# Kernel tuning notes

Measured on AMD Instinct MI355X. Metric: run time of the kernel, lower is better.

Reference implementation:

```python
import jax, jax.numpy as jnp
import numpy as np

NEG_INF = -9.0e15  # matches torch reference's -9e15 masking constant


def setup_inputs() -> dict:
    key = jax.random.key(0)
    k1, k2, k3, k4 = jax.random.split(key, 4)
    N, F_IN, F_OUT = 8192, 256, 256
    x = jax.random.normal(k1, (N, F_IN), dtype=jnp.float32)
    adj = jax.random.randint(k2, (N, N), 0, 2, dtype=jnp.int32)
    W = jax.random.normal(k3, (F_OUT, F_IN), dtype=jnp.float32) * (1.0 / np.sqrt(F_IN))
    a = jax.random.normal(k4, (2 * F_OUT,), dtype=jnp.float32) * (1.0 / np.sqrt(2 * F_OUT))
    return {"x": x, "adj": adj, "W": W, "a": a}


def reference(x, adj, W, a):
    # h = W x  -> [N, F_OUT]
    h = x @ W.T
    F_OUT = h.shape[1]
    # The concat trick: e[i, j] = leaky_relu(a1 . h_i + a2 . h_j)
    # (repeat_interleave gives h_i as the first half, repeat gives h_j as the second half)
    a1, a2 = a[:F_OUT], a[F_OUT:]
    s_i = h @ a1  # [N] -- contribution of destination/row node i
    s_j = h @ a2  # [N] -- contribution of source/col node j
    e = jax.nn.leaky_relu(s_i[:, None] + s_j[None, :], negative_slope=0.2)  # [N, N]
    att = jnp.where(adj > 0, e, jnp.asarray(NEG_INF, dtype=e.dtype))
    att = jax.nn.softmax(att, axis=1)
    # dropout is identity in eval mode / for the deterministic reference
    h_prime = att @ h  # [N, F_OUT]
    return h_prime
```

## Files before the change

kernel.cpp:

```cpp
#include <hip/hip_runtime.h>
#include <hip/hip_bf16.h>

typedef __attribute__((ext_vector_type(4))) float f32x4;
typedef __attribute__((ext_vector_type(8))) short s16x8;
typedef __attribute__((ext_vector_type(4))) int i32x4;
typedef __attribute__((ext_vector_type(4))) unsigned short u16x4;

#define NEG_INF_F (-9.0e15f)
#define LOG2E_F 1.44269504088896340736f
#define N_ROWS 8192
#define F_DIM 256

__device__ __forceinline__ unsigned short f2bf(float f) {
    unsigned int u = __builtin_bit_cast(unsigned int, f);
    u += 0x7fffu + ((u >> 16) & 1u);
    return (unsigned short)(u >> 16);
}

__device__ __forceinline__ float fast_exp2(float x) {
#if __has_builtin(__builtin_amdgcn_exp2f)
    return __builtin_amdgcn_exp2f(x);
#else
    return exp2f(x);
#endif
}

__device__ __forceinline__ short f2bf_fast(float f) {
    __hip_bfloat16 b = __float2bfloat16(f);
    return __builtin_bit_cast(short, b);
}

__global__ __launch_bounds__(256) void k0_pack(const int* __restrict__ adj,
                                               unsigned* __restrict__ mask32) {
    const int t0 = (int)blockIdx.x * 256 + (int)threadIdx.x;
    const int nt = (int)gridDim.x * 256;
#pragma unroll 1
    for (int w = t0; w < (N_ROWS * N_ROWS / 32); w += nt) {
        const int* p = adj + (size_t)w * 32;
        unsigned m = 0;
#pragma unroll
        for (int i = 0; i < 8; ++i) {
            i32x4 v = *(const i32x4*)(p + i * 4);
            m |= (v[0] > 0 ? 1u : 0u) << (i * 4);
            m |= (v[1] > 0 ? 2u : 0u) << (i * 4);
            m |= (v[2] > 0 ? 4u : 0u) << (i * 4);
            m |= (v[3] > 0 ? 8u : 0u) << (i * 4);
        }
        mask32[w] = m;
    }
}

__global__ __launch_bounds__(256) void k1_gemm(const float* __restrict__ x,
                                               const float* __restrict__ W,
                                               unsigned short* __restrict__ hTp) {
    __shared__ float xT[128][64];
    __shared__ float wT[128][64];
    const int tid = threadIdx.x;
    const int rb = blockIdx.x >> 2, fbk = blockIdx.x & 3;
    const int row0 = rb * 64, f0 = fbk * 64;
    const int rs = tid >> 2, cs = tid & 3;
    const int r0 = (tid & 15) * 4, fc = (tid >> 4) * 4;
    float acc[4][4];
#pragma unroll
    for (int i = 0; i < 4; ++i)
#pragma unroll
        for (int j = 0; j < 4; ++j) acc[i][j] = 0.0f;

#pragma unroll 1
    for (int p = 0; p < 2; ++p) {
        const int kb = p * 128;
        if (p) __syncthreads();
        const float* xrow = x + (size_t)(row0 + rs) * F_DIM + kb + cs * 32;
        const float* wrow = W + (size_t)(f0 + rs) * F_DIM + kb + cs * 32;
#pragma unroll
        for (int i = 0; i < 8; ++i) {
            f32x4 xv = *(const f32x4*)(xrow + i * 4);
            f32x4 wv = *(const f32x4*)(wrow + i * 4);
#pragma unroll
            for (int jj = 0; jj < 4; ++jj) {
                xT[cs * 32 + i * 4 + jj][rs] = xv[jj];
                wT[cs * 32 + i * 4 + jj][rs] = wv[jj];
            }
        }
        __syncthreads();
#pragma unroll 4
        for (int kk = 0; kk < 128; ++kk) {
            f32x4 xv = *(const f32x4*)&xT[kk][r0];
            f32x4 wv = *(const f32x4*)&wT[kk][fc];
#pragma unroll
            for (int i = 0; i < 4; ++i)
#pragma unroll
                for (int j = 0; j < 4; ++j)
                    acc[i][j] = fmaf(xv[i], wv[j], acc[i][j]);
        }
    }
    const int kblk = (row0 + r0) >> 3, kslot = (row0 + r0) & 7;
#pragma unroll
    for (int j = 0; j < 4; ++j) {
        u16x4 t;
        t[0] = f2bf(acc[0][j]); t[1] = f2bf(acc[1][j]);
        t[2] = f2bf(acc[2][j]); t[3] = f2bf(acc[3][j]);
        *(u16x4*)(hTp + (size_t)kblk * 2048 + (f0 + fc + j) * 8 + kslot) = t;
    }
}

__global__ __launch_bounds__(256) void kva(const float* __restrict__ W,
                                           const float* __restrict__ a,
                                           float* __restrict__ va) {
    const int k = threadIdx.x;
    const int b = blockIdx.x;
    const float* av = a + b * 256;
    float s0 = 0.f, s1 = 0.f, s2 = 0.f, s3 = 0.f;
#pragma unroll 8
    for (int f = 0; f < 256; f += 4) {
        s0 = fmaf(av[f],     W[(size_t)f * 256 + k],       s0);
        s1 = fmaf(av[f + 1], W[(size_t)(f + 1) * 256 + k], s1);
        s2 = fmaf(av[f + 2], W[(size_t)(f + 2) * 256 + k], s2);
        s3 = fmaf(av[f + 3], W[(size_t)(f + 3) * 256 + k], s3);
    }
    va[b * 256 + k] = (s0 + s1) + (s2 + s3);
}

__global__ __launch_bounds__(256) void k1b_s(const float* __restrict__ x,
                                             const float* __restrict__ va,
                                             float* __restrict__ s1,
                                             float* __restrict__ s2) {
    const int tid = threadIdx.x, lane = tid & 63, w = tid >> 6;
    f32x4 a1 = *(const f32x4*)(va + lane * 4);
    f32x4 a2 = *(const f32x4*)(va + 256 + lane * 4);
    const int row0 = blockIdx.x * 32 + w * 8;
#pragma unroll 1
    for (int rr = 0; rr < 8; ++rr) {
        const int row = row0 + rr;
        f32x4 hv = *(const f32x4*)(x + (size_t)row * F_DIM + lane * 4);
        float p1 = hv[0] * a1[0] + hv[1] * a1[1] + hv[2] * a1[2] + hv[3] * a1[3];
        float p2 = hv[0] * a2[0] + hv[1] * a2[1] + hv[2] * a2[2] + hv[3] * a2[3];
#pragma unroll
        for (int o = 32; o; o >>= 1) { p1 += __shfl_xor(p1, o); p2 += __shfl_xor(p2, o); }
        if (lane == 0) { s1[row] = p1; s2[row] = p2; }
    }
}

__global__ __launch_bounds__(256) void kmax(const unsigned* __restrict__ mask32,
                                            const float* __restrict__ s2,
                                            float* __restrict__ Mrow) {
    __shared__ float s2l[8192];
    const int tid = threadIdx.x, lane = tid & 63, wv = tid >> 6;
#pragma unroll
    for (int i = 0; i < 8; ++i) {
        const int idx = (i * 256 + tid) * 4;
        *(f32x4*)&s2l[idx] = *(const f32x4*)(s2 + idx);
    }
    __syncthreads();
    const int row = (int)blockIdx.x * 4 + wv;
    const unsigned* __restrict__ mr = mask32 + (size_t)row * 256;
    float vmax = NEG_INF_F;
#pragma unroll 1
    for (int wi = 0; wi < 4; ++wi) {
        const unsigned m = mr[lane * 4 + wi];
        const int kb = (lane * 4 + wi) * 32;
#pragma unroll
        for (int cc = 0; cc < 8; ++cc) {
            const int c = (cc + lane) & 7;
            f32x4 v = *(const f32x4*)&s2l[kb + c * 4];
            const unsigned sh = (unsigned)(c * 4);
            vmax = fmaxf(vmax, ((m >> (sh + 0)) & 1u) ? v[0] : NEG_INF_F);
            vmax = fmaxf(vmax, ((m >> (sh + 1)) & 1u) ? v[1] : NEG_INF_F);
            vmax = fmaxf(vmax, ((m >> (sh + 2)) & 1u) ? v[2] : NEG_INF_F);
            vmax = fmaxf(vmax, ((m >> (sh + 3)) & 1u) ? v[3] : NEG_INF_F);
        }
    }
#pragma unroll
    for (int o = 32; o; o >>= 1) vmax = fmaxf(vmax, __shfl_xor(vmax, o));
    if (lane == 0) Mrow[row] = vmax;
}


#define P_ONE(D, SV, BIT, SI, MC)                                             \
    { float t_ = (SI) + (SV); t_ = fmaxf(t_, 0.2f * t_);                      \
      D = fast_exp2(fmaf(((bb_ & (BIT)) ? t_ : NEG_INF_F), LOG2E_F, -(MC))); }

#define RG_STEP(ACC, ACCL, BFR, MW, SI, MC)                                   \
    {                                                                         \
        const unsigned bb_ = ((MW) >> koff) & 0xffu;                          \
        float p0_, p1_, p2_, p3_, p4_, p5_, p6_, p7_;                         \
        P_ONE(p0_, svA_[0], 1u, SI, MC)   P_ONE(p1_, svA_[1], 2u, SI, MC)     \
        P_ONE(p2_, svA_[2], 4u, SI, MC)   P_ONE(p3_, svA_[3], 8u, SI, MC)     \
        P_ONE(p4_, svB_[0], 16u, SI, MC)  P_ONE(p5_, svB_[1], 32u, SI, MC)    \
        P_ONE(p6_, svB_[2], 64u, SI, MC)  P_ONE(p7_, svB_[3], 128u, SI, MC)   \
        s16x8 af_;                                                            \
        af_[0] = f2bf_fast(p0_); af_[1] = f2bf_fast(p1_);                     \
        af_[2] = f2bf_fast(p2_); af_[3] = f2bf_fast(p3_);                     \
        af_[4] = f2bf_fast(p4_); af_[5] = f2bf_fast(p5_);                     \
        af_[6] = f2bf_fast(p6_); af_[7] = f2bf_fast(p7_);                     \
        _Pragma("unroll")                                                     \
        for (int nt_ = 0; nt_ < 8; ++nt_)                                     \
            ACC[nt_] = __builtin_amdgcn_mfma_f32_16x16x32_bf16(af_, BFR[nt_], ACC[nt_], 0, 0, 0); \
        ACCL = __builtin_amdgcn_mfma_f32_16x16x32_bf16(af_, bones, ACCL, 0, 0, 0); \
    }

#define HALF_STEP(BFR, MWA, MWB, K)                                           \
    {                                                                         \
        const f32x4 svA_ = *(const f32x4*)(s2 + (K) + koff);                  \
        const f32x4 svB_ = *(const f32x4*)(s2 + (K) + koff + 4);              \
        RG_STEP(accA, accLA, BFR, MWA, siA, mCA)                              \
        RG_STEP(accB, accLB, BFR, MWB, siB, mCB)                              \
    }

#define LOAD_B(DST, K)                                                        \
    _Pragma("unroll")                                                         \
    for (int nt_ = 0; nt_ < 8; ++nt_)                                         \
        DST[nt_] = *(const s16x8*)(hTp + (unsigned)(((K) >> 3) + kg) * 2048u + vb + (unsigned)(nt_ * 128));

__global__ __launch_bounds__(256) void k2_attn(const unsigned* __restrict__ mask32,
                                               const unsigned short* __restrict__ hTp,
                                               const float* __restrict__ s1,
                                               const float* __restrict__ s2,
                                               const float* __restrict__ Mrow,
                                               float* __restrict__ out) {
    __shared__ float lbuf[4][2][16];
    __shared__ float accbuf[3][16][132];

    const int tid = threadIdx.x;
    const int lane = tid & 63;
    const int wc = tid >> 6;
    const int lane15 = lane & 15, kg = lane >> 4, koff = kg * 8;
    const int rowblk = (int)blockIdx.x >> 1;
    const int fh = (int)blockIdx.x & 1;
    const int row0 = rowblk * 32;
    const int mrowA = row0 + lane15, mrowB = row0 + 16 + lane15;
    const int fb = fh * 128;
    const int kbase = wc * 2048;
    const float siA = s1[mrowA], siB = s1[mrowB];
    const float tmxA = siA + Mrow[mrowA], tmxB = siB + Mrow[mrowB];
    const float mCA = fmaxf(tmxA, 0.2f * tmxA) * LOG2E_F;
    const float mCB = fmaxf(tmxB, 0.2f * tmxB) * LOG2E_F;
    const unsigned* __restrict__ mA32 = mask32 + (size_t)mrowA * 256;
    const unsigned* __restrict__ mB32 = mask32 + (size_t)mrowB * 256;

    f32x4 accA[8], accB[8], accLA, accLB;
#pragma unroll
    for (int nt = 0; nt < 8; ++nt) {
        f32x4 z = {0.f, 0.f, 0.f, 0.f};
        accA[nt] = z; accB[nt] = z;
    }
    { f32x4 z = {0.f, 0.f, 0.f, 0.f}; accLA = z; accLB = z; }

    s16x8 bones;
#pragma unroll
    for (int j = 0; j < 8; ++j) bones[j] = (short)0x3F80;

    const unsigned vb = (unsigned)(fb + lane15) * 8u;

    s16x8 bA[8], bB[8];
    LOAD_B(bA, kbase)
    unsigned mwA = mA32[kbase >> 5], mwB = mB32[kbase >> 5];

#pragma unroll 1
    for (int it = 0; it < 64; it += 2) {
        const int k0 = kbase + it * 32;
        const int k1 = k0 + 32;
        const int k2n = (it + 2 < 64) ? (k0 + 64) : kbase;

        LOAD_B(bB, k1)
        const unsigned mwnA = mA32[k1 >> 5], mwnB = mB32[k1 >> 5];

        HALF_STEP(bA, mwA, mwB, k0);

        LOAD_B(bA, k2n)
        mwA = mA32[k2n >> 5]; mwB = mB32[k2n >> 5];

        HALF_STEP(bB, mwnA, mwnB, k1);
    }

    if (lane15 == 0) {
#pragma unroll
        for (int r = 0; r < 4; ++r) {
            lbuf[wc][0][kg * 4 + r] = accLA[r];
            lbuf[wc][1][kg * 4 + r] = accLB[r];
        }
    }

    if (wc > 0) {
#pragma unroll
        for (int r = 0; r < 4; ++r)
#pragma unroll
            for (int nt = 0; nt < 8; ++nt)
                accbuf[wc - 1][kg * 4 + r][nt * 16 + lane15] = accA[nt][r];
    }
    __syncthreads();
    if (wc == 0) {
#pragma unroll
        for (int r = 0; r < 4; ++r) {
            const int dr = kg * 4 + r;
            const float lt = (lbuf[0][0][dr] + lbuf[1][0][dr]) + (lbuf[2][0][dr] + lbuf[3][0][dr]);
            const float inv = 1.0f / lt;
            float* orow_p = out + (size_t)(row0 + dr) * F_DIM + fb + lane15;
#pragma unroll
            for (int nt = 0; nt < 8; ++nt) {
                const float v = accA[nt][r] + accbuf[0][dr][nt * 16 + lane15]
                              + accbuf[1][dr][nt * 16 + lane15]
                              + accbuf[2][dr][nt * 16 + lane15];
                orow_p[nt * 16] = v * inv;
            }
        }
    }
    __syncthreads();

    if (wc > 0) {
#pragma unroll
        for (int r = 0; r < 4; ++r)
#pragma unroll
            for (int nt = 0; nt < 8; ++nt)
                accbuf[wc - 1][kg * 4 + r][nt * 16 + lane15] = accB[nt][r];
    }
    __syncthreads();
    if (wc == 0) {
#pragma unroll
        for (int r = 0; r < 4; ++r) {
            const int dr = kg * 4 + r;
            const float lt = (lbuf[0][1][dr] + lbuf[1][1][dr]) + (lbuf[2][1][dr] + lbuf[3][1][dr]);
            const float inv = 1.0f / lt;
            float* orow_p = out + (size_t)(row0 + 16 + dr) * F_DIM + fb + lane15;
#pragma unroll
            for (int nt = 0; nt < 8; ++nt) {
                const float v = accB[nt][r] + accbuf[0][dr][nt * 16 + lane15]
                              + accbuf[1][dr][nt * 16 + lane15]
                              + accbuf[2][dr][nt * 16 + lane15];
                orow_p[nt * 16] = v * inv;
            }
        }
    }
}

extern "C" void kernel_launch(void* const* d_in, const int* in_sizes, int n_in,
                              void* d_out, int out_size, void* d_ws, size_t ws_size,
                              hipStream_t stream) {
    (void)in_sizes; (void)n_in; (void)out_size; (void)ws_size;
    const float* x  = (const float*)d_in[0];
    const int*  adj = (const int*)d_in[1];
    const float* W  = (const float*)d_in[2];
    const float* a  = (const float*)d_in[3];
    float* out = (float*)d_out;
    char* ws = (char*)d_ws;
    unsigned short* hTp = (unsigned short*)ws;
    float* s1 = (float*)(ws + (4 << 20));
    float* s2 = (float*)(ws + (4 << 20) + (32 << 10));
    float* va = (float*)(ws + (4 << 20) + (64 << 10));
    float* Mr = (float*)(ws + (4 << 20) + (96 << 10));
    unsigned* mk = (unsigned*)(ws + (4 << 20) + (128 << 10));

    k0_pack<<<2048, 256, 0, stream>>>(adj, mk);
    k1_gemm<<<512, 256, 0, stream>>>(x, W, hTp);
    kva<<<2, 256, 0, stream>>>(W, a, va);
    k1b_s<<<256, 256, 0, stream>>>(x, va, s1, s2);
    kmax<<<2048, 256, 0, stream>>>(mk, s2, Mr);
    k2_attn<<<512, 256, 0, stream>>>(mk, hTp, s1, s2, Mr, out);
}
```

Measured before the change: 180.1 us.

## Factor softmax exponent into per-column and per-row exp tables

Rewrites exp(leaky_relu(s_i+s_j) - m_i) as a product of a per-row constant and a per-column precomputed exponential, choosing the branch by comparing s_j with -s_i. A new small kernel builds two per-column exp tables, exp(s_j) and exp(0.2*s_j), so the inner attention loop replaces one exp2 per element with a select and a multiply. The cost is two extra global vector loads per step, one extra launch, and possible overflow or precision loss when exp(s_j) is computed without the row max.

```diff
diff --git a/kernel.cpp b/kernel.cpp
--- a/kernel.cpp
+++ b/kernel.cpp
@@ -175,19 +175,34 @@
     if (lane == 0) Mrow[row] = vmax;
 }
 
-
-#define P_ONE(D, SV, BIT, SI, MC)                                             \
-    { float t_ = (SI) + (SV); t_ = fmaxf(t_, 0.2f * t_);                      \
-      D = fast_exp2(fmaf(((bb_ & (BIT)) ? t_ : NEG_INF_F), LOG2E_F, -(MC))); }
-
-#define RG_STEP(ACC, ACCL, BFR, MW, SI, MC)                                   \
+__global__ __launch_bounds__(256) void kE(const float* __restrict__ s2,
+                                          float* __restrict__ E1f,
+                                          float* __restrict__ E2f) {
+    const int i = (int)blockIdx.x * 256 + (int)threadIdx.x;
+    const float s = s2[i];
+    E1f[i] = fast_exp2(s * LOG2E_F);
+    E2f[i] = fast_exp2(0.2f * s * LOG2E_F);
+}
+
+
+#define P_ONE(D, SV, E1, E2, BIT, TN, C1, C2)                                 \
+    { const bool cnd_ = (SV) > (TN);                                          \
+      const float e_ = cnd_ ? (E1) : (E2);                                    \
+      const float cc_ = cnd_ ? (C1) : (C2);                                   \
+      D = (bb_ & (BIT)) ? e_ * cc_ : 0.0f; }
+
+#define RG_STEP(ACC, ACCL, BFR, MW, TN, C1, C2)                               \
     {                                                                         \
         const unsigned bb_ = ((MW) >> koff) & 0xffu;                          \
         float p0_, p1_, p2_, p3_, p4_, p5_, p6_, p7_;                         \
-        P_ONE(p0_, svA_[0], 1u, SI, MC)   P_ONE(p1_, svA_[1], 2u, SI, MC)     \
-        P_ONE(p2_, svA_[2], 4u, SI, MC)   P_ONE(p3_, svA_[3], 8u, SI, MC)     \
-        P_ONE(p4_, svB_[0], 16u, SI, MC)  P_ONE(p5_, svB_[1], 32u, SI, MC)    \
-        P_ONE(p6_, svB_[2], 64u, SI, MC)  P_ONE(p7_, svB_[3], 128u, SI, MC)   \
+        P_ONE(p0_, svA_[0], e1A_[0], e2A_[0], 1u,   TN, C1, C2)               \
+        P_ONE(p1_, svA_[1], e1A_[1], e2A_[1], 2u,   TN, C1, C2)               \
+        P_ONE(p2_, svA_[2], e1A_[2], e2A_[2], 4u,   TN, C1, C2)               \
+        P_ONE(p3_, svA_[3], e1A_[3], e2A_[3], 8u,   TN, C1, C2)               \
+        P_ONE(p4_, svB_[0], e1B_[0], e2B_[0], 16u,  TN, C1, C2)               \
+        P_ONE(p5_, svB_[1], e1B_[1], e2B_[1], 32u,  TN, C1, C2)               \
+        P_ONE(p6_, svB_[2], e1B_[2], e2B_[2], 64u,  TN, C1, C2)               \
+        P_ONE(p7_, svB_[3], e1B_[3], e2B_[3], 128u, TN, C1, C2)               \
         s16x8 af_;                                                            \
         af_[0] = f2bf_fast(p0_); af_[1] = f2bf_fast(p1_);                     \
         af_[2] = f2bf_fast(p2_); af_[3] = f2bf_fast(p3_);                     \
@@ -203,8 +218,12 @@
     {                                                                         \
         const f32x4 svA_ = *(const f32x4*)(s2 + (K) + koff);                  \
         const f32x4 svB_ = *(const f32x4*)(s2 + (K) + koff + 4);              \
-        RG_STEP(accA, accLA, BFR, MWA, siA, mCA)                              \
-        RG_STEP(accB, accLB, BFR, MWB, siB, mCB)                              \
+        const f32x4 e1A_ = *(const f32x4*)(E1f + (K) + koff);                 \
+        const f32x4 e1B_ = *(const f32x4*)(E1f + (K) + koff + 4);             \
+        const f32x4 e2A_ = *(const f32x4*)(E2f + (K) + koff);                 \
+        const f32x4 e2B_ = *(const f32x4*)(E2f + (K) + koff + 4);             \
+        RG_STEP(accA, accLA, BFR, MWA, TnA, c1A, c2A)                         \
+        RG_STEP(accB, accLB, BFR, MWB, TnB, c1B, c2B)                         \
     }
 
 #define LOAD_B(DST, K)                                                        \
@@ -217,6 +236,8 @@
                                                const float* __restrict__ s1,
                                                const float* __restrict__ s2,
                                                const float* __restrict__ Mrow,
+                                               const float* __restrict__ E1f,
+                                               const float* __restrict__ E2f,
                                                float* __restrict__ out) {
     __shared__ float lbuf[4][2][16];
     __shared__ float accbuf[3][16][132];
@@ -235,6 +256,11 @@
     const float tmxA = siA + Mrow[mrowA], tmxB = siB + Mrow[mrowB];
     const float mCA = fmaxf(tmxA, 0.2f * tmxA) * LOG2E_F;
     const float mCB = fmaxf(tmxB, 0.2f * tmxB) * LOG2E_F;
+    const float TnA = -siA, TnB = -siB;
+    const float c1A = fast_exp2(fmaf(siA, LOG2E_F, -mCA));
+    const float c2A = fast_exp2(fmaf(0.2f * siA, LOG2E_F, -mCA));
+    const float c1B = fast_exp2(fmaf(siB, LOG2E_F, -mCB));
+    const float c2B = fast_exp2(fmaf(0.2f * siB, LOG2E_F, -mCB));
     const unsigned* __restrict__ mA32 = mask32 + (size_t)mrowA * 256;
     const unsigned* __restrict__ mB32 = mask32 + (size_t)mrowB * 256;
 
@@ -348,12 +374,15 @@
     float* s2 = (float*)(ws + (4 << 20) + (32 << 10));
     float* va = (float*)(ws + (4 << 20) + (64 << 10));
     float* Mr = (float*)(ws + (4 << 20) + (96 << 10));
-    unsigned* mk = (unsigned*)(ws + (4 << 20) + (128 << 10));
+    float* E1 = (float*)(ws + (4 << 20) + (128 << 10));
+    float* E2 = (float*)(ws + (4 << 20) + (160 << 10));
+    unsigned* mk = (unsigned*)(ws + (4 << 20) + (192 << 10));
 
     k0_pack<<<2048, 256, 0, stream>>>(adj, mk);
     k1_gemm<<<512, 256, 0, stream>>>(x, W, hTp);
     kva<<<2, 256, 0, stream>>>(W, a, va);
     k1b_s<<<256, 256, 0, stream>>>(x, va, s1, s2);
     kmax<<<2048, 256, 0, stream>>>(mk, s2, Mr);
-    k2_attn<<<512, 256, 0, stream>>>(mk, hTp, s1, s2, Mr, out);
-}
+    kE<<<32, 256, 0, stream>>>(s2, E1, E2);
+    k2_attn<<<512, 256, 0, stream>>>(mk, hTp, s1, s2, Mr, E1, E2, out);
+}
```

Measured after the change: 212.5 us. +18.0%, slower.

## Widen attention tile to 64 rows and split K across two launches

Applied to the files above, without the earlier changes.

Each attention block now handles 64 rows instead of 32, so every loaded hT B-fragment feeds four row groups of MFMAs rather than two, halving B traffic per unit of work. The K range is split into two kernel launches of 256 blocks. The first writes partial numerators and denominators, and the second adds its partials and normalises. This doubles accumulator registers, which may lower occupancy or cause spills, and adds a read-modify-write of the output between launches.

```diff
diff --git a/kernel.cpp b/kernel.cpp
--- a/kernel.cpp
+++ b/kernel.cpp
@@ -199,12 +199,14 @@
         ACCL = __builtin_amdgcn_mfma_f32_16x16x32_bf16(af_, bones, ACCL, 0, 0, 0); \
     }
 
-#define HALF_STEP(BFR, MWA, MWB, K)                                           \
+#define HALF_STEP(BFR, MWA, MWB, MWC, MWD, K)                                 \
     {                                                                         \
         const f32x4 svA_ = *(const f32x4*)(s2 + (K) + koff);                  \
         const f32x4 svB_ = *(const f32x4*)(s2 + (K) + koff + 4);              \
         RG_STEP(accA, accLA, BFR, MWA, siA, mCA)                              \
         RG_STEP(accB, accLB, BFR, MWB, siB, mCB)                              \
+        RG_STEP(accC, accLC, BFR, MWC, siC, mCC)                              \
+        RG_STEP(accD, accLD, BFR, MWD, siD, mCD)                              \
     }
 
 #define LOAD_B(DST, K)                                                        \
@@ -212,13 +214,55 @@
     for (int nt_ = 0; nt_ < 8; ++nt_)                                         \
         DST[nt_] = *(const s16x8*)(hTp + (unsigned)(((K) >> 3) + kg) * 2048u + vb + (unsigned)(nt_ * 128));
 
+#define OUT_PHASE(ACC, RG, RGOFF)                                             \
+    if (wc > 0) {                                                             \
+        _Pragma("unroll")                                                     \
+        for (int r = 0; r < 4; ++r)                                           \
+            _Pragma("unroll")                                                 \
+            for (int nt = 0; nt < 8; ++nt)                                    \
+                accbuf[wc - 1][kg * 4 + r][nt * 16 + lane15] = ACC[nt][r];    \
+    }                                                                         \
+    __syncthreads();                                                          \
+    if (wc == 0) {                                                            \
+        _Pragma("unroll")                                                     \
+        for (int r = 0; r < 4; ++r) {                                         \
+            const int dr = kg * 4 + r;                                        \
+            const int row = row0 + (RGOFF) + dr;                              \
+            const float lt = (lbuf[0][RG][dr] + lbuf[1][RG][dr])              \
+                           + (lbuf[2][RG][dr] + lbuf[3][RG][dr]);             \
+            float* orow_p = out + (size_t)row * F_DIM + fb + lane15;          \
+            if (ADD) {                                                        \
+                const float inv = 1.0f / (Lp[row] + lt);                      \
+                _Pragma("unroll")                                             \
+                for (int nt = 0; nt < 8; ++nt) {                              \
+                    const float v = ACC[nt][r] + accbuf[0][dr][nt * 16 + lane15] \
+                                  + accbuf[1][dr][nt * 16 + lane15]           \
+                                  + accbuf[2][dr][nt * 16 + lane15];          \
+                    orow_p[nt * 16] = (orow_p[nt * 16] + v) * inv;            \
+                }                                                             \
+            } else {                                                          \
+                _Pragma("unroll")                                             \
+                for (int nt = 0; nt < 8; ++nt) {                              \
+                    const float v = ACC[nt][r] + accbuf[0][dr][nt * 16 + lane15] \
+                                  + accbuf[1][dr][nt * 16 + lane15]           \
+                                  + accbuf[2][dr][nt * 16 + lane15];          \
+                    orow_p[nt * 16] = v;                                      \
+                }                                                             \
+                if (fh == 0 && lane15 == 0) Lp[row] = lt;                     \
+            }                                                                 \
+        }                                                                     \
+    }                                                                         \
+    __syncthreads();
+
+template <int ADD>
 __global__ __launch_bounds__(256) void k2_attn(const unsigned* __restrict__ mask32,
                                                const unsigned short* __restrict__ hTp,
                                                const float* __restrict__ s1,
                                                const float* __restrict__ s2,
                                                const float* __restrict__ Mrow,
+                                               float* __restrict__ Lp,
                                                float* __restrict__ out) {
-    __shared__ float lbuf[4][2][16];
+    __shared__ float lbuf[4][4][16];
     __shared__ float accbuf[3][16][132];
 
     const int tid = threadIdx.x;
@@ -227,24 +271,31 @@
     const int lane15 = lane & 15, kg = lane >> 4, koff = kg * 8;
     const int rowblk = (int)blockIdx.x >> 1;
     const int fh = (int)blockIdx.x & 1;
-    const int row0 = rowblk * 32;
-    const int mrowA = row0 + lane15, mrowB = row0 + 16 + lane15;
+    const int row0 = rowblk * 64;
+    const int mrowA = row0 + lane15,      mrowB = row0 + 16 + lane15;
+    const int mrowC = row0 + 32 + lane15, mrowD = row0 + 48 + lane15;
     const int fb = fh * 128;
-    const int kbase = wc * 2048;
+    const int kbase = ADD * 4096 + wc * 1024;
     const float siA = s1[mrowA], siB = s1[mrowB];
+    const float siC = s1[mrowC], siD = s1[mrowD];
     const float tmxA = siA + Mrow[mrowA], tmxB = siB + Mrow[mrowB];
+    const float tmxC = siC + Mrow[mrowC], tmxD = siD + Mrow[mrowD];
     const float mCA = fmaxf(tmxA, 0.2f * tmxA) * LOG2E_F;
     const float mCB = fmaxf(tmxB, 0.2f * tmxB) * LOG2E_F;
+    const float mCC = fmaxf(tmxC, 0.2f * tmxC) * LOG2E_F;
+    const float mCD = fmaxf(tmxD, 0.2f * tmxD) * LOG2E_F;
     const unsigned* __restrict__ mA32 = mask32 + (size_t)mrowA * 256;
     const unsigned* __restrict__ mB32 = mask32 + (size_t)mrowB * 256;
-
-    f32x4 accA[8], accB[8], accLA, accLB;
+    const unsigned* __restrict__ mC32 = mask32 + (size_t)mrowC * 256;
+    const unsigned* __restrict__ mD32 = mask32 + (size_t)mrowD * 256;
+
+    f32x4 accA[8], accB[8], accC[8], accD[8], accLA, accLB, accLC, accLD;
 #pragma unroll
     for (int nt = 0; nt < 8; ++nt) {
         f32x4 z = {0.f, 0.f, 0.f, 0.f};
-        accA[nt] = z; accB[nt] = z;
-    }
-    { f32x4 z = {0.f, 0.f, 0.f, 0.f}; accLA = z; accLB = z; }
+        accA[nt] = z; accB[nt] = z; accC[nt] = z; accD[nt] = z;
+    }
+    { f32x4 z = {0.f, 0.f, 0.f, 0.f}; accLA = z; accLB = z; accLC = z; accLD = z; }
 
     s16x8 bones;
 #pragma unroll
@@ -255,22 +306,25 @@
     s16x8 bA[8], bB[8];
     LOAD_B(bA, kbase)
     unsigned mwA = mA32[kbase >> 5], mwB = mB32[kbase >> 5];
-
-#pragma unroll 1
-    for (int it = 0; it < 64; it += 2) {
+    unsigned mwC = mC32[kbase >> 5], mwD = mD32[kbase >> 5];
+
+#pragma unroll 1
+    for (int it = 0; it < 32; it += 2) {
         const int k0 = kbase + it * 32;
         const int k1 = k0 + 32;
-        const int k2n = (it + 2 < 64) ? (k0 + 64) : kbase;
+        const int k2n = (it + 2 < 32) ? (k0 + 64) : kbase;
 
         LOAD_B(bB, k1)
         const unsigned mwnA = mA32[k1 >> 5], mwnB = mB32[k1 >> 5];
-
-        HALF_STEP(bA, mwA, mwB, k0);
+        const unsigned mwnC = mC32[k1 >> 5], mwnD = mD32[k1 >> 5];
+
+        HALF_STEP(bA, mwA, mwB, mwC, mwD, k0);
 
         LOAD_B(bA, k2n)
         mwA = mA32[k2n >> 5]; mwB = mB32[k2n >> 5];
-
-        HALF_STEP(bB, mwnA, mwnB, k1);
+        mwC = mC32[k2n >> 5]; mwD = mD32[k2n >> 5];
+
+        HALF_STEP(bB, mwnA, mwnB, mwnC, mwnD, k1);
     }
 
     if (lane15 == 0) {
@@ -278,59 +332,15 @@
         for (int r = 0; r < 4; ++r) {
             lbuf[wc][0][kg * 4 + r] = accLA[r];
             lbuf[wc][1][kg * 4 + r] = accLB[r];
-        }
-    }
-
-    if (wc > 0) {
-#pragma unroll
-        for (int r = 0; r < 4; ++r)
-#pragma unroll
-            for (int nt = 0; nt < 8; ++nt)
-                accbuf[wc - 1][kg * 4 + r][nt * 16 + lane15] = accA[nt][r];
-    }
-    __syncthreads();
-    if (wc == 0) {
-#pragma unroll
-        for (int r = 0; r < 4; ++r) {
-            const int dr = kg * 4 + r;
-            const float lt = (lbuf[0][0][dr] + lbuf[1][0][dr]) + (lbuf[2][0][dr] + lbuf[3][0][dr]);
-            const float inv = 1.0f / lt;
-            float* orow_p = out + (size_t)(row0 + dr) * F_DIM + fb + lane15;
-#pragma unroll
-            for (int nt = 0; nt < 8; ++nt) {
-                const float v = accA[nt][r] + accbuf[0][dr][nt * 16 + lane15]
-                              + accbuf[1][dr][nt * 16 + lane15]
-                              + accbuf[2][dr][nt * 16 + lane15];
-                orow_p[nt * 16] = v * inv;
-            }
-        }
-    }
-    __syncthreads();
-
-    if (wc > 0) {
-#pragma unroll
-        for (int r = 0; r < 4; ++r)
-#pragma unroll
-            for (int nt = 0; nt < 8; ++nt)
-                accbuf[wc - 1][kg * 4 + r][nt * 16 + lane15] = accB[nt][r];
-    }
-    __syncthreads();
-    if (wc == 0) {
-#pragma unroll
-        for (int r = 0; r < 4; ++r) {
-            const int dr = kg * 4 + r;
-            const float lt = (lbuf[0][1][dr] + lbuf[1][1][dr]) + (lbuf[2][1][dr] + lbuf[3][1][dr]);
-            const float inv = 1.0f / lt;
-            float* orow_p = out + (size_t)(row0 + 16 + dr) * F_DIM + fb + lane15;
-#pragma unroll
-            for (int nt = 0; nt < 8; ++nt) {
-                const float v = accB[nt][r] + accbuf[0][dr][nt * 16 + lane15]
-                              + accbuf[1][dr][nt * 16 + lane15]
-                              + accbuf[2][dr][nt * 16 + lane15];
-                orow_p[nt * 16] = v * inv;
-            }
-        }
-    }
+            lbuf[wc][2][kg * 4 + r] = accLC[r];
+            lbuf[wc][3][kg * 4 + r] = accLD[r];
+        }
+    }
+
+    OUT_PHASE(accA, 0, 0)
+    OUT_PHASE(accB, 1, 16)
+    OUT_PHASE(accC, 2, 32)
+    OUT_PHASE(accD, 3, 48)
 }
 
 extern "C" void kernel_launch(void* const* d_in, const int* in_sizes, int n_in,
@@ -348,12 +358,14 @@
     float* s2 = (float*)(ws + (4 << 20) + (32 << 10));
     float* va = (float*)(ws + (4 << 20) + (64 << 10));
     float* Mr = (float*)(ws + (4 << 20) + (96 << 10));
-    unsigned* mk = (unsigned*)(ws + (4 << 20) + (128 << 10));
+    float* Lp = (float*)(ws + (4 << 20) + (128 << 10));
+    unsigned* mk = (unsigned*)(ws + (4 << 20) + (160 << 10));
 
     k0_pack<<<2048, 256, 0, stream>>>(adj, mk);
     k1_gemm<<<512, 256, 0, stream>>>(x, W, hTp);
     kva<<<2, 256, 0, stream>>>(W, a, va);
     k1b_s<<<256, 256, 0, stream>>>(x, va, s1, s2);
     kmax<<<2048, 256, 0, stream>>>(mk, s2, Mr);
-    k2_attn<<<512, 256, 0, stream>>>(mk, hTp, s1, s2, Mr, out);
-}
+    k2_attn<0><<<256, 256, 0, stream>>>(mk, hTp, s1, s2, Mr, Lp, out);
+    k2_attn<1><<<256, 256, 0, stream>>>(mk, hTp, s1, s2, Mr, Lp, out);
+}
```

After: 189.1 us. 1.05x slower.
